# Optimization experiments

Hardware: AMD Instinct MI355X
Metric: run time of the kernel (lower is better)

Reference implementation:

```python
import jax, jax.numpy as jnp
import numpy as np

N, B, FIN, E, EDIM, H, C = 20000, 2, 256, 320000, 64, 8, 32


def setup_inputs() -> dict:
    key = jax.random.key(0)
    ks = jax.random.split(key, 12)
    s = 1.0 / np.sqrt(FIN)
    se = 1.0 / np.sqrt(EDIM)
    return {
        "x": jax.random.normal(ks[0], (N, B, FIN), jnp.float32),
        "edata": jax.random.normal(ks[1], (E, EDIM), jnp.float32),
        "edge_src": jax.random.randint(ks[2], (E,), 0, N, jnp.int32),
        "edge_dst": jax.random.randint(ks[3], (E,), 0, N, jnp.int32),
        "Wq": jax.random.normal(ks[4], (FIN, H * C), jnp.float32) * s,
        "bq": jnp.zeros((H * C,), jnp.float32),
        "Wk": jax.random.normal(ks[5], (FIN, H * C), jnp.float32) * s,
        "bk": jnp.zeros((H * C,), jnp.float32),
        "Wv": jax.random.normal(ks[6], (FIN, H * C), jnp.float32) * s,
        "bv": jnp.zeros((H * C,), jnp.float32),
        "We": jax.random.normal(ks[7], (EDIM, H * C), jnp.float32) * se,
        "Wr": jax.random.normal(ks[8], (FIN, H * C), jnp.float32) * s,
        "br": jnp.zeros((H * C,), jnp.float32),
    }


def reference(x, edata, edge_src, edge_dst, Wq, bq, Wk, bk, Wv, bv, We, Wr, br):
    # x: [N, B, FIN]; edata: [E, EDIM]
    q = (x @ Wq + bq).reshape(N, B, H, C)   # dst queries
    k = (x @ Wk + bk).reshape(N, B, H, C)   # src keys
    v = (x @ Wv + bv).reshape(N, B, H, C)   # src values
    e = (edata @ We).reshape(E, 1, H, C)    # edge feats, broadcast over batch

    scale = 1.0 / np.sqrt(C)
    # per-edge logits: (u_mul_v / sqrt(C) + edata).sum(-1) -> [E, B, H]
    logits = (k[edge_src] * q[edge_dst] * scale + e).sum(-1)

    # edge_softmax over edges sharing the same destination node
    m = jax.ops.segment_max(logits, edge_dst, num_segments=N)      # [N, B, H]
    ex = jnp.exp(logits - m[edge_dst])
    z = jax.ops.segment_sum(ex, edge_dst, num_segments=N)          # [N, B, H]
    alpha = ex / z[edge_dst]                                       # [E, B, H]

    # weighted scatter-sum aggregation: u_mul_e + sum over dst
    att_v = v[edge_src] * alpha[..., None]                         # [E, B, H, C]
    agg = jax.ops.segment_sum(att_v, edge_dst, num_segments=N)     # [N, B, H, C]

    out = agg.reshape(N, B, H * C) + (x @ Wr + br)
    return out
```

## Files before the change

kernel.cpp:

```cpp
#include <hip/hip_runtime.h>
#include <hip/hip_bf16.h>

#define NN    20000
#define BB    2
#define EE    320000
#define MROWS (NN * BB)

typedef __bf16 bf16x8 __attribute__((ext_vector_type(8)));
typedef float  floatx4 __attribute__((ext_vector_type(4)));


__global__ __launch_bounds__(256) void prep_kernel(
    const float* __restrict__ Wq, const float* __restrict__ Wk,
    const float* __restrict__ Wv, const float* __restrict__ Wr,
    __hip_bfloat16* __restrict__ wt,
    const float* __restrict__ bq, const float* __restrict__ bk,
    const float* __restrict__ bv, const float* __restrict__ br,
    float* __restrict__ bcat,
    const float* __restrict__ We, float* __restrict__ wesum,
    const int* __restrict__ edst, int* __restrict__ counts) {
  __shared__ float TA[32][65];
  __shared__ float TB[32][65];
  int bt = blockIdx.x;
  int t = threadIdx.x;

  if (bt < 16) {
    const float *A, *B;
    int c0, jbase;
    if (bt < 8) { A = Wk; B = Wv; c0 = 32 * bt;      jbase = 64 * bt; }
    else        { A = Wq; B = Wr; c0 = 32 * (bt-8);  jbase = 512 + 64 * (bt-8); }
    int krow = t >> 2;
    int cc = (t & 3) * 8;
    int sel = t >> 7;
    int u = t & 127;
    int ci = u >> 2;
    int kk0 = (u & 3) * 16;

    for (int kt = 0; kt < 4; ++kt) {
      int k = kt * 64 + krow;
      float4 a0 = *(const float4*)(A + (size_t)k * 256 + c0 + cc);
      float4 a1 = *(const float4*)(A + (size_t)k * 256 + c0 + cc + 4);
      float4 b0 = *(const float4*)(B + (size_t)k * 256 + c0 + cc);
      float4 b1 = *(const float4*)(B + (size_t)k * 256 + c0 + cc + 4);
      __syncthreads();
      TA[cc+0][krow]=a0.x; TA[cc+1][krow]=a0.y; TA[cc+2][krow]=a0.z; TA[cc+3][krow]=a0.w;
      TA[cc+4][krow]=a1.x; TA[cc+5][krow]=a1.y; TA[cc+6][krow]=a1.z; TA[cc+7][krow]=a1.w;
      TB[cc+0][krow]=b0.x; TB[cc+1][krow]=b0.y; TB[cc+2][krow]=b0.z; TB[cc+3][krow]=b0.w;
      TB[cc+4][krow]=b1.x; TB[cc+5][krow]=b1.y; TB[cc+6][krow]=b1.z; TB[cc+7][krow]=b1.w;
      __syncthreads();
      float (*T)[65] = sel ? TB : TA;
      int j = jbase + 2 * ci + sel;
      __hip_bfloat16* dst = wt + (size_t)j * 256 + kt * 64 + kk0;
      #pragma unroll
      for (int q = 0; q < 16; ++q) dst[q] = __float2bfloat16(T[ci][kk0 + q]);
    }
  } else if (bt == 16) {
    #pragma unroll
    for (int jj = 0; jj < 4; ++jj) {
      int j = jj * 256 + t;
      float val;
      if (j < 512) { int c = j >> 1;         val = (j & 1) ? bv[c] : bk[c]; }
      else         { int c = (j - 512) >> 1; val = (j & 1) ? br[c] : bq[c]; }
      bcat[j] = val;
    }
    #pragma unroll
    for (int ii = 0; ii < 2; ++ii) {
      int i = ii * 256 + t;
      int h = i >> 6, d = i & 63;
      float s = 0.f;
      for (int c = 0; c < 32; ++c) s += We[(size_t)d * 256 + h * 32 + c];
      wesum[h * 64 + d] = s;
    }
  } else {
    int e = (bt - 17) * 256 + t;
    if (e < EE) atomicAdd(&counts[edst[e]], 1);
  }
}

__global__ void scan_kernel(const int* __restrict__ counts,
                            int* __restrict__ offsets,
                            int* __restrict__ cursor) {
  __shared__ int part[256];
  int t = threadIdx.x;
  const int per = (NN + 255) / 256;
  int lo = t * per, hi = min(lo + per, NN);
  int s = 0;
  #pragma unroll 4
  for (int i = lo; i < hi; ++i) s += counts[i];
  part[t] = s;
  __syncthreads();
  for (int off = 1; off < 256; off <<= 1) {
    int v = (t >= off) ? part[t - off] : 0;
    __syncthreads();
    part[t] += v;
    __syncthreads();
  }
  int base = (t == 0) ? 0 : part[t - 1];
  for (int i = lo; i < hi; ++i) {
    offsets[i] = base;
    cursor[i] = base;
    base += counts[i];
  }
  if (t == 255) offsets[NN] = base;
}

__global__ __launch_bounds__(256) void scatter_esum(
    const int* __restrict__ edst, const int* __restrict__ esrc,
    int* __restrict__ cursor,
    const float* __restrict__ edata, const float* __restrict__ wesum,
    int* __restrict__ ssrc, float* __restrict__ esum) {
  __shared__ float wl[512];
  int t = threadIdx.x;
  wl[t] = wesum[t];
  wl[t + 256] = wesum[t + 256];
  __syncthreads();
  int e = blockIdx.x * 256 + t;
  int p = atomicAdd(&cursor[edst[e]], 1);
  ssrc[p] = esrc[e];
  float acc[8] = {};
  const float* row = edata + (size_t)e * 64;
  for (int d = 0; d < 64; d += 4) {
    float4 v = *(const float4*)(row + d);
    #pragma unroll
    for (int hh = 0; hh < 8; ++hh) {
      const float* wv = &wl[hh * 64 + d];
      acc[hh] += v.x * wv[0] + v.y * wv[1] + v.z * wv[2] + v.w * wv[3];
    }
  }
  float* op = esum + (size_t)p * 8;
  *(float4*)op       = make_float4(acc[0], acc[1], acc[2], acc[3]);
  *(float4*)(op + 4) = make_float4(acc[4], acc[5], acc[6], acc[7]);
}

__global__ __launch_bounds__(256) void gemm_qkvr(
    const float* __restrict__ x,
    const __bf16* __restrict__ wt,
    const float* __restrict__ bcat,
    __hip_bfloat16* __restrict__ out) {
  const int LSTR = 40;
  __shared__ __attribute__((aligned(16))) __bf16 As[64 * LSTR];
  __shared__ __attribute__((aligned(16))) __bf16 Bs[256 * LSTR];

  int m0 = blockIdx.y * 64;
  int n0 = blockIdx.x * 256;
  int t = threadIdx.x;
  int w = t >> 6, l = t & 63;
  int lr = l & 15, lq = l >> 4;
  int ar = t >> 2, ac = (t & 3) * 8;

  floatx4 acc[4][4] = {};

  for (int ks = 0; ks < 8; ++ks) {
    const float* xp = x + (size_t)(m0 + ar) * 256 + ks * 32 + ac;
    float4 f0 = *(const float4*)xp;
    float4 f1 = *(const float4*)(xp + 4);
    bf16x8 av;
    av[0] = (__bf16)f0.x; av[1] = (__bf16)f0.y;
    av[2] = (__bf16)f0.z; av[3] = (__bf16)f0.w;
    av[4] = (__bf16)f1.x; av[5] = (__bf16)f1.y;
    av[6] = (__bf16)f1.z; av[7] = (__bf16)f1.w;
    const __bf16* wp = wt + (size_t)(n0 + t) * 256 + ks * 32;
    bf16x8 b0 = *(const bf16x8*)(wp);
    bf16x8 b1 = *(const bf16x8*)(wp + 8);
    bf16x8 b2 = *(const bf16x8*)(wp + 16);
    bf16x8 b3 = *(const bf16x8*)(wp + 24);
    __syncthreads();
    *(bf16x8*)&As[ar * LSTR + ac] = av;
    __bf16* bsr = &Bs[t * LSTR];
    *(bf16x8*)(bsr)      = b0;
    *(bf16x8*)(bsr + 8)  = b1;
    *(bf16x8*)(bsr + 16) = b2;
    *(bf16x8*)(bsr + 24) = b3;
    __syncthreads();
    bf16x8 af[4], bf_[4];
    #pragma unroll
    for (int mt = 0; mt < 4; ++mt)
      af[mt] = *(const bf16x8*)&As[(16 * mt + lr) * LSTR + lq * 8];
    #pragma unroll
    for (int nt = 0; nt < 4; ++nt)
      bf_[nt] = *(const bf16x8*)&Bs[(64 * w + 16 * nt + lr) * LSTR + lq * 8];
    #pragma unroll
    for (int mt = 0; mt < 4; ++mt)
      #pragma unroll
      for (int nt = 0; nt < 4; ++nt)
        acc[mt][nt] = __builtin_amdgcn_mfma_f32_16x16x32_bf16(af[mt], bf_[nt], acc[mt][nt], 0, 0, 0);
  }

  #pragma unroll
  for (int mt = 0; mt < 4; ++mt)
    #pragma unroll
    for (int nt = 0; nt < 4; ++nt)
      #pragma unroll
      for (int r = 0; r < 4; ++r) {
        int gr = m0 + 16 * mt + lq * 4 + r;
        int gc = n0 + 64 * w + 16 * nt + lr;
        out[(size_t)gr * 1024 + gc] = __float2bfloat16(acc[mt][nt][r] + bcat[gc]);
      }
}

#define LOADSLOT(K0, K1, EV, IDX)                                    \
  { int s_ = __builtin_amdgcn_readlane(s_l, (IDX));                  \
    const unsigned* p_ = kvl + (size_t)s_ * 1024;                    \
    K0 = *(const uint4*)p_;                                          \
    K1 = *(const uint4*)(p_ + 512);                                  \
    EV = esp[(size_t)(IDX) * 8]; }

#define CONSUME(K0, K1, EV)                                          \
  { float pa = __uint_as_float(K0.x << 16) * qa0                     \
             + __uint_as_float(K0.y << 16) * qa1                     \
             + __uint_as_float(K0.z << 16) * qa2                     \
             + __uint_as_float(K0.w << 16) * qa3;                    \
    float pb = __uint_as_float(K1.x << 16) * qb0                     \
             + __uint_as_float(K1.y << 16) * qb1                     \
             + __uint_as_float(K1.z << 16) * qb2                     \
             + __uint_as_float(K1.w << 16) * qb3;                    \
    pa += __shfl_xor(pa, 1, 64);  pb += __shfl_xor(pb, 1, 64);       \
    pa += __shfl_xor(pa, 2, 64);  pb += __shfl_xor(pb, 2, 64);       \
    pa += __shfl_xor(pa, 4, 64);  pb += __shfl_xor(pb, 4, 64);       \
    float ea_ = __expf(pa * 0.17677669529663687f + EV);              \
    float eb_ = __expf(pb * 0.17677669529663687f + EV);              \
    za += ea_; zb += eb_;                                            \
    aa0 += ea_ * __uint_as_float(K0.x & 0xFFFF0000u);                \
    aa1 += ea_ * __uint_as_float(K0.y & 0xFFFF0000u);                \
    aa2 += ea_ * __uint_as_float(K0.z & 0xFFFF0000u);                \
    aa3 += ea_ * __uint_as_float(K0.w & 0xFFFF0000u);                \
    ab0 += eb_ * __uint_as_float(K1.x & 0xFFFF0000u);                \
    ab1 += eb_ * __uint_as_float(K1.y & 0xFFFF0000u);                \
    ab2 += eb_ * __uint_as_float(K1.z & 0xFFFF0000u);                \
    ab3 += eb_ * __uint_as_float(K1.w & 0xFFFF0000u); }

__global__ __launch_bounds__(256) void aggregate_kernel(
    const unsigned int* __restrict__ qkvr,
    const float* __restrict__ esum,
    const int* __restrict__ offsets,
    const int* __restrict__ ssrc,
    float* __restrict__ out) {
  int t = threadIdx.x;
  int w = t >> 6, l = t & 63;
  int n = blockIdx.x * 4 + w;
  int h = l >> 3;
  int beg = offsets[n], end = offsets[n + 1];

  uint4 qra = *(const uint4*)(qkvr + (size_t)(2 * n) * 512 + 256 + l * 4);
  uint4 qrb = *(const uint4*)(qkvr + (size_t)(2 * n + 1) * 512 + 256 + l * 4);
  float qa0 = __uint_as_float(qra.x << 16), qa1 = __uint_as_float(qra.y << 16);
  float qa2 = __uint_as_float(qra.z << 16), qa3 = __uint_as_float(qra.w << 16);
  float qb0 = __uint_as_float(qrb.x << 16), qb1 = __uint_as_float(qrb.y << 16);
  float qb2 = __uint_as_float(qrb.z << 16), qb3 = __uint_as_float(qrb.w << 16);

  const unsigned* kvl = qkvr + l * 4;

  float za = 0.f, zb = 0.f;
  float aa0 = 0.f, aa1 = 0.f, aa2 = 0.f, aa3 = 0.f;
  float ab0 = 0.f, ab1 = 0.f, ab2 = 0.f, ab3 = 0.f;

  for (int base = beg; base < end; base += 64) {
    int chunk = min(64, end - base);
    int s_l = (l < chunk) ? ssrc[base + l] : 0;
    const float* esp = esum + (size_t)base * 8 + h;
    uint4 kA0 = {0,0,0,0}, kA1 = {0,0,0,0}, kB0 = {0,0,0,0}, kB1 = {0,0,0,0};
    uint4 kC0 = {0,0,0,0}, kC1 = {0,0,0,0}, kD0 = {0,0,0,0}, kD1 = {0,0,0,0};
    float eA = 0.f, eB = 0.f, eC = 0.f, eD = 0.f;
    LOADSLOT(kA0, kA1, eA, 0);
    if (chunk > 1) LOADSLOT(kB0, kB1, eB, 1);
    if (chunk > 2) LOADSLOT(kC0, kC1, eC, 2);
    if (chunk > 3) LOADSLOT(kD0, kD1, eD, 3);
    for (int i = 0; i < chunk; i += 4) {
      CONSUME(kA0, kA1, eA);
      if (i + 4 < chunk) LOADSLOT(kA0, kA1, eA, i + 4);
      if (i + 1 < chunk) {
        CONSUME(kB0, kB1, eB);
        if (i + 5 < chunk) LOADSLOT(kB0, kB1, eB, i + 5);
        if (i + 2 < chunk) {
          CONSUME(kC0, kC1, eC);
          if (i + 6 < chunk) LOADSLOT(kC0, kC1, eC, i + 6);
          if (i + 3 < chunk) {
            CONSUME(kD0, kD1, eD);
            if (i + 7 < chunk) LOADSLOT(kD0, kD1, eD, i + 7);
          }
        }
      }
    }
  }
  float ia = (za > 0.f) ? 1.f / za : 0.f;
  float ib = (zb > 0.f) ? 1.f / zb : 0.f;
  float4 oa = make_float4(aa0 * ia + __uint_as_float(qra.x & 0xFFFF0000u),
                          aa1 * ia + __uint_as_float(qra.y & 0xFFFF0000u),
                          aa2 * ia + __uint_as_float(qra.z & 0xFFFF0000u),
                          aa3 * ia + __uint_as_float(qra.w & 0xFFFF0000u));
  float4 ob = make_float4(ab0 * ib + __uint_as_float(qrb.x & 0xFFFF0000u),
                          ab1 * ib + __uint_as_float(qrb.y & 0xFFFF0000u),
                          ab2 * ib + __uint_as_float(qrb.z & 0xFFFF0000u),
                          ab3 * ib + __uint_as_float(qrb.w & 0xFFFF0000u));
  *(float4*)(out + (size_t)(2 * n) * 256 + l * 4) = oa;
  *(float4*)(out + (size_t)(2 * n + 1) * 256 + l * 4) = ob;
}

extern "C" void kernel_launch(void* const* d_in, const int* in_sizes, int n_in,
                              void* d_out, int out_size, void* d_ws, size_t ws_size,
                              hipStream_t stream) {
  (void)in_sizes; (void)n_in; (void)out_size; (void)ws_size;
  const float* x     = (const float*)d_in[0];
  const float* edata = (const float*)d_in[1];
  const int* esrc    = (const int*)d_in[2];
  const int* edst    = (const int*)d_in[3];
  const float* Wq    = (const float*)d_in[4];
  const float* bq    = (const float*)d_in[5];
  const float* Wk    = (const float*)d_in[6];
  const float* bk    = (const float*)d_in[7];
  const float* Wv    = (const float*)d_in[8];
  const float* bv    = (const float*)d_in[9];
  const float* We    = (const float*)d_in[10];
  const float* Wr    = (const float*)d_in[11];
  const float* br    = (const float*)d_in[12];
  float* out = (float*)d_out;

  char* ws = (char*)d_ws;
  size_t off = 0;
  auto carve = [&](size_t bytes) -> void* {
    void* p = ws + off;
    off += (bytes + 255) & ~(size_t)255;
    return p;
  };
  int* counts    = (int*)carve((size_t)NN * 4);
  int* offsets   = (int*)carve((size_t)(NN + 1) * 4);
  int* cursor    = (int*)carve((size_t)NN * 4);
  int* ssrc      = (int*)carve((size_t)EE * 4);
  __hip_bfloat16* wt = (__hip_bfloat16*)carve((size_t)1024 * 256 * 2);
  float* bcat    = (float*)carve(1024 * 4);
  float* wesum   = (float*)carve(8 * 64 * 4);
  float* esum    = (float*)carve((size_t)EE * 8 * 4);
  __hip_bfloat16* qkvr = (__hip_bfloat16*)carve((size_t)MROWS * 1024 * 2);

  hipMemsetAsync(counts, 0, (size_t)NN * 4, stream);
  prep_kernel<<<17 + (EE + 255) / 256, 256, 0, stream>>>(
      Wq, Wk, Wv, Wr, wt, bq, bk, bv, br, bcat, We, wesum, edst, counts);
  scan_kernel<<<1, 256, 0, stream>>>(counts, offsets, cursor);
  scatter_esum<<<EE / 256, 256, 0, stream>>>(edst, esrc, cursor, edata, wesum,
                                             ssrc, esum);
  gemm_qkvr<<<dim3(4, 625), 256, 0, stream>>>(x, (const __bf16*)wt, bcat, qkvr);
  aggregate_kernel<<<NN / 4, 256, 0, stream>>>((const unsigned int*)qkvr, esum,
                                               offsets, ssrc, out);
}
```

Before: 428.0 us.

## Pre-convert x to bf16, deepen GEMM K-tile, split aggregation per batch

Measured after the change: 416.8 us. 1.03x faster.

```diff
diff --git a/kernel.cpp b/kernel.cpp
--- a/kernel.cpp
+++ b/kernel.cpp
@@ -7,8 +7,12 @@
 #define MROWS (NN * BB)
 
 typedef __bf16 bf16x8 __attribute__((ext_vector_type(8)));
+typedef __bf16 bf16x4 __attribute__((ext_vector_type(4)));
 typedef float  floatx4 __attribute__((ext_vector_type(4)));
 
+
+#define NB_HIST 1250
+#define NB_CVT  1250
 
 __global__ __launch_bounds__(256) void prep_kernel(
     const float* __restrict__ Wq, const float* __restrict__ Wk,
@@ -18,7 +22,8 @@
     const float* __restrict__ bv, const float* __restrict__ br,
     float* __restrict__ bcat,
     const float* __restrict__ We, float* __restrict__ wesum,
-    const int* __restrict__ edst, int* __restrict__ counts) {
+    const int* __restrict__ edst, int* __restrict__ counts,
+    const float* __restrict__ x, __bf16* __restrict__ xb) {
   __shared__ float TA[32][65];
   __shared__ float TB[32][65];
   int bt = blockIdx.x;
@@ -71,9 +76,20 @@
       for (int c = 0; c < 32; ++c) s += We[(size_t)d * 256 + h * 32 + c];
       wesum[h * 64 + d] = s;
     }
-  } else {
+  } else if (bt < 17 + NB_HIST) {
     int e = (bt - 17) * 256 + t;
     if (e < EE) atomicAdd(&counts[edst[e]], 1);
+  } else {
+    int cb = bt - 17 - NB_HIST;
+    size_t base = (size_t)cb * 8192 + t * 4;
+    #pragma unroll
+    for (int j = 0; j < 8; ++j) {
+      float4 v = *(const float4*)(x + base + j * 1024);
+      bf16x4 o;
+      o[0] = (__bf16)v.x; o[1] = (__bf16)v.y;
+      o[2] = (__bf16)v.z; o[3] = (__bf16)v.w;
+      *(bf16x4*)(xb + base + j * 1024) = o;
+    }
   }
 }
 
@@ -133,11 +149,11 @@
 }
 
 __global__ __launch_bounds__(256) void gemm_qkvr(
-    const float* __restrict__ x,
+    const __bf16* __restrict__ xb,
     const __bf16* __restrict__ wt,
     const float* __restrict__ bcat,
     __hip_bfloat16* __restrict__ out) {
-  const int LSTR = 40;
+  const int LSTR = 72;
   __shared__ __attribute__((aligned(16))) __bf16 As[64 * LSTR];
   __shared__ __attribute__((aligned(16))) __bf16 Bs[256 * LSTR];
 
@@ -146,44 +162,51 @@
   int t = threadIdx.x;
   int w = t >> 6, l = t & 63;
   int lr = l & 15, lq = l >> 4;
-  int ar = t >> 2, ac = (t & 3) * 8;
+  int ar = t >> 2, ac = (t & 3) * 16;
 
   floatx4 acc[4][4] = {};
 
-  for (int ks = 0; ks < 8; ++ks) {
-    const float* xp = x + (size_t)(m0 + ar) * 256 + ks * 32 + ac;
-    float4 f0 = *(const float4*)xp;
-    float4 f1 = *(const float4*)(xp + 4);
-    bf16x8 av;
-    av[0] = (__bf16)f0.x; av[1] = (__bf16)f0.y;
-    av[2] = (__bf16)f0.z; av[3] = (__bf16)f0.w;
-    av[4] = (__bf16)f1.x; av[5] = (__bf16)f1.y;
-    av[6] = (__bf16)f1.z; av[7] = (__bf16)f1.w;
-    const __bf16* wp = wt + (size_t)(n0 + t) * 256 + ks * 32;
+  for (int ks = 0; ks < 4; ++ks) {
+    const __bf16* xp = xb + (size_t)(m0 + ar) * 256 + ks * 64 + ac;
+    bf16x8 a0 = *(const bf16x8*)xp;
+    bf16x8 a1 = *(const bf16x8*)(xp + 8);
+    const __bf16* wp = wt + (size_t)(n0 + t) * 256 + ks * 64;
     bf16x8 b0 = *(const bf16x8*)(wp);
     bf16x8 b1 = *(const bf16x8*)(wp + 8);
     bf16x8 b2 = *(const bf16x8*)(wp + 16);
     bf16x8 b3 = *(const bf16x8*)(wp + 24);
+    bf16x8 b4 = *(const bf16x8*)(wp + 32);
+    bf16x8 b5 = *(const bf16x8*)(wp + 40);
+    bf16x8 b6 = *(const bf16x8*)(wp + 48);
+    bf16x8 b7 = *(const bf16x8*)(wp + 56);
     __syncthreads();
-    *(bf16x8*)&As[ar * LSTR + ac] = av;
+    *(bf16x8*)&As[ar * LSTR + ac]     = a0;
+    *(bf16x8*)&As[ar * LSTR + ac + 8] = a1;
     __bf16* bsr = &Bs[t * LSTR];
     *(bf16x8*)(bsr)      = b0;
     *(bf16x8*)(bsr + 8)  = b1;
     *(bf16x8*)(bsr + 16) = b2;
     *(bf16x8*)(bsr + 24) = b3;
+    *(bf16x8*)(bsr + 32) = b4;
+    *(bf16x8*)(bsr + 40) = b5;
+    *(bf16x8*)(bsr + 48) = b6;
+    *(bf16x8*)(bsr + 56) = b7;
     __syncthreads();
-    bf16x8 af[4], bf_[4];
-    #pragma unroll
-    for (int mt = 0; mt < 4; ++mt)
-      af[mt] = *(const bf16x8*)&As[(16 * mt + lr) * LSTR + lq * 8];
-    #pragma unroll
-    for (int nt = 0; nt < 4; ++nt)
-      bf_[nt] = *(const bf16x8*)&Bs[(64 * w + 16 * nt + lr) * LSTR + lq * 8];
-    #pragma unroll
-    for (int mt = 0; mt < 4; ++mt)
+    #pragma unroll
+    for (int kk = 0; kk < 2; ++kk) {
+      bf16x8 af[4], bf_[4];
+      #pragma unroll
+      for (int mt = 0; mt < 4; ++mt)
+        af[mt] = *(const bf16x8*)&As[(16 * mt + lr) * LSTR + kk * 32 + lq * 8];
       #pragma unroll
       for (int nt = 0; nt < 4; ++nt)
-        acc[mt][nt] = __builtin_amdgcn_mfma_f32_16x16x32_bf16(af[mt], bf_[nt], acc[mt][nt], 0, 0, 0);
+        bf_[nt] = *(const bf16x8*)&Bs[(64 * w + 16 * nt + lr) * LSTR + kk * 32 + lq * 8];
+      #pragma unroll
+      for (int mt = 0; mt < 4; ++mt)
+        #pragma unroll
+        for (int nt = 0; nt < 4; ++nt)
+          acc[mt][nt] = __builtin_amdgcn_mfma_f32_16x16x32_bf16(af[mt], bf_[nt], acc[mt][nt], 0, 0, 0);
+    }
   }
 
   #pragma unroll
@@ -198,36 +221,25 @@
       }
 }
 
-#define LOADSLOT(K0, K1, EV, IDX)                                    \
+#define LOADSLOT(KV, EV, IDX)                                        \
   { int s_ = __builtin_amdgcn_readlane(s_l, (IDX));                  \
-    const unsigned* p_ = kvl + (size_t)s_ * 1024;                    \
-    K0 = *(const uint4*)p_;                                          \
-    K1 = *(const uint4*)(p_ + 512);                                  \
+    KV = *(const uint4*)(kvl + (size_t)s_ * 1024);                   \
     EV = esp[(size_t)(IDX) * 8]; }
 
-#define CONSUME(K0, K1, EV)                                          \
-  { float pa = __uint_as_float(K0.x << 16) * qa0                     \
-             + __uint_as_float(K0.y << 16) * qa1                     \
-             + __uint_as_float(K0.z << 16) * qa2                     \
-             + __uint_as_float(K0.w << 16) * qa3;                    \
-    float pb = __uint_as_float(K1.x << 16) * qb0                     \
-             + __uint_as_float(K1.y << 16) * qb1                     \
-             + __uint_as_float(K1.z << 16) * qb2                     \
-             + __uint_as_float(K1.w << 16) * qb3;                    \
-    pa += __shfl_xor(pa, 1, 64);  pb += __shfl_xor(pb, 1, 64);       \
-    pa += __shfl_xor(pa, 2, 64);  pb += __shfl_xor(pb, 2, 64);       \
-    pa += __shfl_xor(pa, 4, 64);  pb += __shfl_xor(pb, 4, 64);       \
-    float ea_ = __expf(pa * 0.17677669529663687f + EV);              \
-    float eb_ = __expf(pb * 0.17677669529663687f + EV);              \
-    za += ea_; zb += eb_;                                            \
-    aa0 += ea_ * __uint_as_float(K0.x & 0xFFFF0000u);                \
-    aa1 += ea_ * __uint_as_float(K0.y & 0xFFFF0000u);                \
-    aa2 += ea_ * __uint_as_float(K0.z & 0xFFFF0000u);                \
-    aa3 += ea_ * __uint_as_float(K0.w & 0xFFFF0000u);                \
-    ab0 += eb_ * __uint_as_float(K1.x & 0xFFFF0000u);                \
-    ab1 += eb_ * __uint_as_float(K1.y & 0xFFFF0000u);                \
-    ab2 += eb_ * __uint_as_float(K1.z & 0xFFFF0000u);                \
-    ab3 += eb_ * __uint_as_float(K1.w & 0xFFFF0000u); }
+#define CONSUME(KV, EV)                                              \
+  { float part = __uint_as_float(KV.x << 16) * q0                    \
+               + __uint_as_float(KV.y << 16) * q1                    \
+               + __uint_as_float(KV.z << 16) * q2                    \
+               + __uint_as_float(KV.w << 16) * q3;                   \
+    part += __shfl_xor(part, 1, 64);                                 \
+    part += __shfl_xor(part, 2, 64);                                 \
+    part += __shfl_xor(part, 4, 64);                                 \
+    float p = __expf(part * 0.17677669529663687f + EV);              \
+    z += p;                                                          \
+    a0 += p * __uint_as_float(KV.x & 0xFFFF0000u);                   \
+    a1 += p * __uint_as_float(KV.y & 0xFFFF0000u);                   \
+    a2 += p * __uint_as_float(KV.z & 0xFFFF0000u);                   \
+    a3 += p * __uint_as_float(KV.w & 0xFFFF0000u); }
 
 __global__ __launch_bounds__(256) void aggregate_kernel(
     const unsigned int* __restrict__ qkvr,
@@ -237,63 +249,63 @@
     float* __restrict__ out) {
   int t = threadIdx.x;
   int w = t >> 6, l = t & 63;
-  int n = blockIdx.x * 4 + w;
+  int nb = blockIdx.x * 4 + w;
+  int b = nb & 1, n = nb >> 1;
   int h = l >> 3;
   int beg = offsets[n], end = offsets[n + 1];
 
-  uint4 qra = *(const uint4*)(qkvr + (size_t)(2 * n) * 512 + 256 + l * 4);
-  uint4 qrb = *(const uint4*)(qkvr + (size_t)(2 * n + 1) * 512 + 256 + l * 4);
-  float qa0 = __uint_as_float(qra.x << 16), qa1 = __uint_as_float(qra.y << 16);
-  float qa2 = __uint_as_float(qra.z << 16), qa3 = __uint_as_float(qra.w << 16);
-  float qb0 = __uint_as_float(qrb.x << 16), qb1 = __uint_as_float(qrb.y << 16);
-  float qb2 = __uint_as_float(qrb.z << 16), qb3 = __uint_as_float(qrb.w << 16);
-
-  const unsigned* kvl = qkvr + l * 4;
-
-  float za = 0.f, zb = 0.f;
-  float aa0 = 0.f, aa1 = 0.f, aa2 = 0.f, aa3 = 0.f;
-  float ab0 = 0.f, ab1 = 0.f, ab2 = 0.f, ab3 = 0.f;
+  uint4 qr4 = *(const uint4*)(qkvr + (size_t)nb * 512 + 256 + l * 4);
+  float q0 = __uint_as_float(qr4.x << 16), q1 = __uint_as_float(qr4.y << 16);
+  float q2 = __uint_as_float(qr4.z << 16), q3 = __uint_as_float(qr4.w << 16);
+
+  const unsigned* kvl = qkvr + (size_t)b * 512 + l * 4;
+
+  float z = 0.f, a0 = 0.f, a1 = 0.f, a2 = 0.f, a3 = 0.f;
 
   for (int base = beg; base < end; base += 64) {
     int chunk = min(64, end - base);
     int s_l = (l < chunk) ? ssrc[base + l] : 0;
     const float* esp = esum + (size_t)base * 8 + h;
-    uint4 kA0 = {0,0,0,0}, kA1 = {0,0,0,0}, kB0 = {0,0,0,0}, kB1 = {0,0,0,0};
-    uint4 kC0 = {0,0,0,0}, kC1 = {0,0,0,0}, kD0 = {0,0,0,0}, kD1 = {0,0,0,0};
-    float eA = 0.f, eB = 0.f, eC = 0.f, eD = 0.f;
-    LOADSLOT(kA0, kA1, eA, 0);
-    if (chunk > 1) LOADSLOT(kB0, kB1, eB, 1);
-    if (chunk > 2) LOADSLOT(kC0, kC1, eC, 2);
-    if (chunk > 3) LOADSLOT(kD0, kD1, eD, 3);
-    for (int i = 0; i < chunk; i += 4) {
-      CONSUME(kA0, kA1, eA);
-      if (i + 4 < chunk) LOADSLOT(kA0, kA1, eA, i + 4);
+    uint4 k0 = {0,0,0,0}, k1 = {0,0,0,0}, k2 = {0,0,0,0};
+    uint4 k3 = {0,0,0,0}, k4 = {0,0,0,0}, k5 = {0,0,0,0};
+    float e0 = 0.f, e1 = 0.f, e2 = 0.f, e3 = 0.f, e4 = 0.f, e5 = 0.f;
+    LOADSLOT(k0, e0, 0);
+    if (chunk > 1) LOADSLOT(k1, e1, 1);
+    if (chunk > 2) LOADSLOT(k2, e2, 2);
+    if (chunk > 3) LOADSLOT(k3, e3, 3);
+    if (chunk > 4) LOADSLOT(k4, e4, 4);
+    if (chunk > 5) LOADSLOT(k5, e5, 5);
+    for (int i = 0; i < chunk; i += 6) {
+      CONSUME(k0, e0);
+      if (i + 6 < chunk) LOADSLOT(k0, e0, i + 6);
       if (i + 1 < chunk) {
-        CONSUME(kB0, kB1, eB);
-        if (i + 5 < chunk) LOADSLOT(kB0, kB1, eB, i + 5);
+        CONSUME(k1, e1);
+        if (i + 7 < chunk) LOADSLOT(k1, e1, i + 7);
         if (i + 2 < chunk) {
-          CONSUME(kC0, kC1, eC);
-          if (i + 6 < chunk) LOADSLOT(kC0, kC1, eC, i + 6);
+          CONSUME(k2, e2);
+          if (i + 8 < chunk) LOADSLOT(k2, e2, i + 8);
           if (i + 3 < chunk) {
-            CONSUME(kD0, kD1, eD);
-            if (i + 7 < chunk) LOADSLOT(kD0, kD1, eD, i + 7);
+            CONSUME(k3, e3);
+            if (i + 9 < chunk) LOADSLOT(k3, e3, i + 9);
+            if (i + 4 < chunk) {
+              CONSUME(k4, e4);
+              if (i + 10 < chunk) LOADSLOT(k4, e4, i + 10);
+              if (i + 5 < chunk) {
+                CONSUME(k5, e5);
+                if (i + 11 < chunk) LOADSLOT(k5, e5, i + 11);
+              }
+            }
           }
         }
       }
     }
   }
-  float ia = (za > 0.f) ? 1.f / za : 0.f;
-  float ib = (zb > 0.f) ? 1.f / zb : 0.f;
-  float4 oa = make_float4(aa0 * ia + __uint_as_float(qra.x & 0xFFFF0000u),
-                          aa1 * ia + __uint_as_float(qra.y & 0xFFFF0000u),
-                          aa2 * ia + __uint_as_float(qra.z & 0xFFFF0000u),
-                          aa3 * ia + __uint_as_float(qra.w & 0xFFFF0000u));
-  float4 ob = make_float4(ab0 * ib + __uint_as_float(qrb.x & 0xFFFF0000u),
-                          ab1 * ib + __uint_as_float(qrb.y & 0xFFFF0000u),
-                          ab2 * ib + __uint_as_float(qrb.z & 0xFFFF0000u),
-                          ab3 * ib + __uint_as_float(qrb.w & 0xFFFF0000u));
-  *(float4*)(out + (size_t)(2 * n) * 256 + l * 4) = oa;
-  *(float4*)(out + (size_t)(2 * n + 1) * 256 + l * 4) = ob;
+  float inv = (z > 0.f) ? (1.0f / z) : 0.f;
+  float4 o = make_float4(a0 * inv + __uint_as_float(qr4.x & 0xFFFF0000u),
+                         a1 * inv + __uint_as_float(qr4.y & 0xFFFF0000u),
+                         a2 * inv + __uint_as_float(qr4.z & 0xFFFF0000u),
+                         a3 * inv + __uint_as_float(qr4.w & 0xFFFF0000u));
+  *(float4*)(out + (size_t)nb * 256 + l * 4) = o;
 }
 
 extern "C" void kernel_launch(void* const* d_in, const int* in_sizes, int n_in,
@@ -330,15 +342,16 @@
   float* bcat    = (float*)carve(1024 * 4);
   float* wesum   = (float*)carve(8 * 64 * 4);
   float* esum    = (float*)carve((size_t)EE * 8 * 4);
+  __bf16* xb     = (__bf16*)carve((size_t)MROWS * 256 * 2);
   __hip_bfloat16* qkvr = (__hip_bfloat16*)carve((size_t)MROWS * 1024 * 2);
 
   hipMemsetAsync(counts, 0, (size_t)NN * 4, stream);
-  prep_kernel<<<17 + (EE + 255) / 256, 256, 0, stream>>>(
-      Wq, Wk, Wv, Wr, wt, bq, bk, bv, br, bcat, We, wesum, edst, counts);
+  prep_kernel<<<17 + NB_HIST + NB_CVT, 256, 0, stream>>>(
+      Wq, Wk, Wv, Wr, wt, bq, bk, bv, br, bcat, We, wesum, edst, counts, x, xb);
   scan_kernel<<<1, 256, 0, stream>>>(counts, offsets, cursor);
   scatter_esum<<<EE / 256, 256, 0, stream>>>(edst, esrc, cursor, edata, wesum,
                                              ssrc, esum);
-  gemm_qkvr<<<dim3(4, 625), 256, 0, stream>>>(x, (const __bf16*)wt, bcat, qkvr);
-  aggregate_kernel<<<NN / 4, 256, 0, stream>>>((const unsigned int*)qkvr, esum,
-                                               offsets, ssrc, out);
-}
+  gemm_qkvr<<<dim3(4, 625), 256, 0, stream>>>(xb, (const __bf16*)wt, bcat, qkvr);
+  aggregate_kernel<<<MROWS / 4, 256, 0, stream>>>((const unsigned int*)qkvr, esum,
+                                                  offsets, ssrc, out);
+}
```
